# Performance work log

Hardware: AMD Instinct MI355X
Metric: run time of the kernel (lower is better)

Reference implementation:

```python
import jax, jax.numpy as jnp
import numpy as np

N_HEAD = 12


def setup_inputs() -> dict:
    key = jax.random.key(0)
    k1, k2, k3, k4 = jax.random.split(key, 4)
    B, T, C = 2, 2048, 768
    x = jax.random.normal(k1, (B, T, C), jnp.float32)
    eps = 0.1 * jnp.abs(jax.random.normal(k2, (B, T, C), jnp.float32))
    return {
        "x": x,
        "x_lower": x - eps,
        "x_upper": x + eps,
        "W_attn": 0.02 * jax.random.normal(k3, (3 * C, C), jnp.float32),
        "W_proj": 0.02 * jax.random.normal(k4, (C, C), jnp.float32),
    }


def _sdpa(q, k, v):
    # q,k,v: [B,H,T,D]; causal softmax attention
    T = q.shape[-2]
    scale = 1.0 / np.sqrt(q.shape[-1]).astype(np.float32)
    att = jnp.einsum('bhqd,bhkd->bhqk', q, k) * scale
    mask = jnp.tril(jnp.ones((T, T), dtype=bool))
    att = jnp.where(mask, att, -jnp.inf)
    att = jax.nn.softmax(att, axis=-1)
    return jnp.einsum('bhqk,bhkd->bhqd', att, v)


def reference(x, x_lower, x_upper, W_attn, W_proj):
    B, T, C = x.shape
    H = N_HEAD
    D = C // H

    def qkv(inp, W):
        out = inp @ W.T  # [B,T,3C]
        q, k, v = jnp.split(out, 3, axis=-1)
        hd = lambda t: t.reshape(B, T, H, D).transpose(0, 2, 1, 3)
        return hd(q), hd(k), hd(v)

    # nominal path
    q, k, v = qkv(x, W_attn)

    # signed weight split: positive keeps W>=0 entries, negative keeps W<0
    Wp = jnp.maximum(W_attn, 0.0)
    Wn = jnp.minimum(W_attn, 0.0)

    qup, kup, vup = qkv(x_upper, Wp)
    qun, kun, vun = qkv(x_upper, Wn)
    qlp, klp, vlp = qkv(x_lower, Wp)
    qln, kln, vln = qkv(x_lower, Wn)

    q_lo, q_hi = qlp + qun, qup + qln
    k_lo, k_hi = klp + kun, kup + kln
    v_lo, v_hi = vlp + vun, vup + vln

    y = _sdpa(q, k, v)
    # 8 interval-bound SDPA branches (q outer, k mid, v inner: lll..uuu)
    combos = [
        _sdpa(qa, ka, va)
        for qa in (q_lo, q_hi)
        for ka in (k_lo, k_hi)
        for va in (v_lo, v_hi)
    ]
    y_all = jnp.stack(combos, axis=0)  # [8,B,H,T,D]
    y_lo = y_all.min(axis=0)
    y_hi = y_all.max(axis=0)

    merge = lambda t: t.transpose(0, 2, 1, 3).reshape(B, T, C)
    return (merge(y) @ W_proj.T, merge(y_lo) @ W_proj.T, merge(y_hi) @ W_proj.T)
```

## Files before the change

kernel.cpp:

```cpp
#include <hip/hip_runtime.h>
#include <hip/hip_bf16.h>
#include <cstdint>

typedef float f4  __attribute__((ext_vector_type(4)));
typedef short s8v __attribute__((ext_vector_type(8)));
typedef int   i4v __attribute__((ext_vector_type(4)));

#define BHTD 3145728
#define BTC  3145728
#define NT   2048
#define NC   768
#define NWA  1769472
#define NEG  -1e30f
#define QSCALE 0.18033688f

static __device__ __forceinline__ short bfbits(float f) {
    return __builtin_bit_cast(short, __float2bfloat16(f));
}
static __device__ __forceinline__ float bf2f(short s) {
    return __builtin_bit_cast(float, (int)(((unsigned int)(unsigned short)s) << 16));
}
static __device__ __forceinline__ float exp2fast(float x) {
    return __builtin_amdgcn_exp2f(x);
}
static __device__ __forceinline__ int cvtpk_bf16(float lo, float hi) {
    int r;
    asm("v_cvt_pk_bf16_f32 %0, %1, %2" : "=v"(r) : "v"(lo), "v"(hi));
    return r;
}
static __device__ __forceinline__ float rowred_max(float x) {
    x = fmaxf(x, __shfl_xor(x, 16, 64));
    x = fmaxf(x, __shfl_xor(x, 32, 64));
    return x;
}
static __device__ __forceinline__ float rowred_sum(float x) {
    x += __shfl_xor(x, 16, 64);
    x += __shfl_xor(x, 32, 64);
    return x;
}

__global__ __launch_bounds__(256) void prep_cvt(
    const float* __restrict__ x, const float* __restrict__ xl,
    const float* __restrict__ xu, const float* __restrict__ W,
    short* __restrict__ xn, short* __restrict__ xm, short* __restrict__ xr,
    short* __restrict__ wb)
{
    const size_t flat = (size_t)blockIdx.x * 256 + threadIdx.x;
    const size_t i = flat * 8;
    {
        const f4 a0 = *(const f4*)&x[i],  a1 = *(const f4*)&x[i + 4];
        const f4 l0 = *(const f4*)&xl[i], l1 = *(const f4*)&xl[i + 4];
        const f4 u0 = *(const f4*)&xu[i], u1 = *(const f4*)&xu[i + 4];
        s8v vn, vm, vr;
#pragma unroll
        for (int j = 0; j < 4; j++) {
            vn[j]     = bfbits(a0[j]);                   vn[4 + j] = bfbits(a1[j]);
            vm[j]     = bfbits(0.5f * (l0[j] + u0[j]));  vm[4 + j] = bfbits(0.5f * (l1[j] + u1[j]));
            vr[j]     = bfbits(0.5f * (u0[j] - l0[j]));  vr[4 + j] = bfbits(0.5f * (u1[j] - l1[j]));
        }
        *(s8v*)&xn[i] = vn;
        *(s8v*)&xm[i] = vm;
        *(s8v*)&xr[i] = vr;
    }
    if (flat < NWA / 8) {
        const size_t wi = flat * 8;
        const f4 w0 = *(const f4*)&W[wi], w1 = *(const f4*)&W[wi + 4];
        s8v vw;
#pragma unroll
        for (int j = 0; j < 4; j++) { vw[j] = bfbits(w0[j]); vw[4 + j] = bfbits(w1[j]); }
        *(s8v*)&wb[wi] = vw;
    }
}

__global__ __launch_bounds__(256) void qkv_proj_mfma(
    const short* __restrict__ xn, const short* __restrict__ xm,
    const short* __restrict__ xr, const short* __restrict__ wb,
    short* __restrict__ qkvb)
{
    __shared__ short sm[2][4 * 2560];
    short* Eb = &sm[0][0];

    const int b_  = blockIdx.x;
    const int xcd = b_ & 7;
    const int s_  = b_ >> 3;
    const int jx  = s_ % 36;
    const int ny  = xcd + 8 * (s_ / 36);
    const int j0 = jx * 64;
    const int n0 = ny * 64;
    const int t  = threadIdx.x;
    const int wv = t >> 6, lane = t & 63, quad = lane >> 4, l16 = lane & 15;
    const int rw = t >> 2, koff = (t & 3) * 8;

    f4 aN[4], aM[4], aR[4];
#pragma unroll
    for (int i = 0; i < 4; i++) { aN[i] = f4{0,0,0,0}; aM[i] = f4{0,0,0,0}; aR[i] = f4{0,0,0,0}; }

    const size_t abase = (size_t)(n0 + rw) * NC + koff;
    const size_t bbase = (size_t)(j0 + rw) * NC + koff;

    s8v rn, rm, rr, rb;
    rn = *(const s8v*)&xn[abase];
    rm = *(const s8v*)&xm[abase];
    rr = *(const s8v*)&xr[abase];
    rb = *(const s8v*)&wb[bbase];
    *(s8v*)&sm[0][rw * 40 + koff]        = rn;
    *(s8v*)&sm[0][2560 + rw * 40 + koff] = rm;
    *(s8v*)&sm[0][5120 + rw * 40 + koff] = rr;
    *(s8v*)&sm[0][7680 + rw * 40 + koff] = rb;

    for (int it = 0; it < NC / 32; ++it) {
        const int cb = it & 1, nb = cb ^ 1;
        __syncthreads();
        const bool pf = (it + 1 < NC / 32);
        if (pf) {
            const size_t k1 = (size_t)(it + 1) * 32;
            rn = *(const s8v*)&xn[abase + k1];
            rm = *(const s8v*)&xm[abase + k1];
            rr = *(const s8v*)&xr[abase + k1];
            rb = *(const s8v*)&wb[bbase + k1];
        }
        const s8v fx = *(const s8v*)&sm[cb][(wv * 16 + l16) * 40 + quad * 8];
        const s8v fm = *(const s8v*)&sm[cb][2560 + (wv * 16 + l16) * 40 + quad * 8];
        const s8v fr = *(const s8v*)&sm[cb][5120 + (wv * 16 + l16) * 40 + quad * 8];
#pragma unroll
        for (int nt = 0; nt < 4; ++nt) {
            const s8v fb = *(const s8v*)&sm[cb][7680 + (nt * 16 + l16) * 40 + quad * 8];
            i4v bi = __builtin_bit_cast(i4v, fb);
#pragma unroll
            for (int i = 0; i < 4; i++) bi[i] &= 0x7fff7fff;
            const s8v fa = __builtin_bit_cast(s8v, bi);
            aN[nt] = __builtin_amdgcn_mfma_f32_16x16x32_bf16(fx, fb, aN[nt], 0, 0, 0);
            aM[nt] = __builtin_amdgcn_mfma_f32_16x16x32_bf16(fm, fb, aM[nt], 0, 0, 0);
            aR[nt] = __builtin_amdgcn_mfma_f32_16x16x32_bf16(fr, fa, aR[nt], 0, 0, 0);
        }
        if (pf) {
            *(s8v*)&sm[nb][rw * 40 + koff]        = rn;
            *(s8v*)&sm[nb][2560 + rw * 40 + koff] = rm;
            *(s8v*)&sm[nb][5120 + rw * 40 + koff] = rr;
            *(s8v*)&sm[nb][7680 + rw * 40 + koff] = rb;
        }
    }

    const int p = j0 / NC, hh = (j0 % NC) >> 6;
    const float osc = (p == 0) ? QSCALE : 1.0f;
    const int cc16 = (t & 3) * 16;
    for (int var = 0; var < 3; ++var) {
        __syncthreads();
#pragma unroll
        for (int nt = 0; nt < 4; ++nt)
#pragma unroll
            for (int r = 0; r < 4; ++r) {
                const float v = (var == 0) ? aN[nt][r]
                              : (var == 1) ? aM[nt][r] - aR[nt][r]
                                           : aM[nt][r] + aR[nt][r];
                Eb[(wv * 16 + quad * 4 + r) * 72 + nt * 16 + l16] = bfbits(v * osc);
            }
        __syncthreads();
        short* dst = qkvb + (size_t)(var * 3 + p) * BHTD;
        if (p < 2) {
            const int token = n0 + rw, b = token >> 11, tt = token & 2047;
            const size_t o = ((size_t)(b * 12 + hh) * NT + tt) * 64 + cc16;
            *(s8v*)&dst[o]     = *(const s8v*)&Eb[rw * 72 + cc16];
            *(s8v*)&dst[o + 8] = *(const s8v*)&Eb[rw * 72 + cc16 + 8];
        } else {
            const int d = rw;
            s8v e0, e1;
#pragma unroll
            for (int i = 0; i < 8; i++) e0[i] = Eb[(cc16 + i) * 72 + d];
#pragma unroll
            for (int i = 0; i < 8; i++) e1[i] = Eb[(cc16 + 8 + i) * 72 + d];
            const int token0 = n0 + cc16, b = token0 >> 11, tt = token0 & 2047;
            const size_t o = ((size_t)(b * 12 + hh) * 64 + d) * NT + tt;
            *(s8v*)&dst[o]     = e0;
            *(s8v*)&dst[o + 8] = e1;
        }
    }
}

__global__ __launch_bounds__(256) void flash_mfma(
    const short* __restrict__ qkvb, float* __restrict__ ybuf,
    short* __restrict__ cand)
{
    const int b_  = blockIdx.x;
    const int xcd = b_ & 7;
    const int r_  = b_ >> 3;
    const int pr  = r_ & 7;
    const int r2  = r_ >> 3;
    const int z   = r2 % 5;
    const int bh  = xcd + 8 * (r2 / 5);
    const int t   = threadIdx.x;
    const int wv = t >> 6, lane = t & 63, quad = lane >> 4, l16 = lane & 15;
    const bool TWO = (z != 0);

    __shared__ short Ks[2][32 * 70];
    __shared__ short Vs[2][2][64 * 40];

    int sv, qvi, kvi, v0i, v1i;
    if (TWO) { sv = z; qvi = (sv + 1) >> 1; kvi = 2 - (sv & 1); v0i = 1; v1i = 2; }
    else     { sv = 0; qvi = 0; kvi = 0; v0i = 0; v1i = 0; }

    const size_t hb = (size_t)bh * (NT * 64);
    const short* Qp  = qkvb + (size_t)(qvi * 3 + 0) * BHTD + hb;
    const short* Kp  = qkvb + (size_t)(kvi * 3 + 1) * BHTD + hb;
    const short* V0p = qkvb + (size_t)(v0i * 3 + 2) * BHTD + hb;
    const short* V1p = qkvb + (size_t)(v1i * 3 + 2) * BHTD + hb;

    const int skr = t >> 3, skc = (t & 7) * 8;
    const int svd = t >> 2, svc = (t & 3) * 8;
    const int sig = (l16 >> 2) * 8 + (l16 & 3);

    for (int half = 0; half < 2; ++half) {
        const int qt = half ? (15 - pr) : pr;
        const int q0 = qt * 128;

        s8v qf[2][2];
#pragma unroll
        for (int mt = 0; mt < 2; ++mt)
#pragma unroll
            for (int ch = 0; ch < 2; ++ch)
                qf[mt][ch] = *(const s8v*)&Qp[(size_t)(q0 + 32 * wv + 16 * mt + l16) * 64 + ch * 32 + quad * 8];

        float mi[2], li[2];
        mi[0] = mi[1] = NEG; li[0] = li[1] = 0.f;
        f4 acc0[2][4], acc1[2][4];
#pragma unroll
        for (int mt = 0; mt < 2; ++mt)
#pragma unroll
            for (int i = 0; i < 4; ++i) { acc0[mt][i] = f4{0,0,0,0}; acc1[mt][i] = f4{0,0,0,0}; }

        const int ktn  = 4 * qt + 4;
        const int mykt = 4 * qt + wv + 1;

        __syncthreads();
        s8v rK, rV0, rV1;
        rK  = *(const s8v*)&Kp[(size_t)skr * 64 + skc];
        rV0 = *(const s8v*)&V0p[(size_t)svd * NT + svc];
        if (TWO) rV1 = *(const s8v*)&V1p[(size_t)svd * NT + svc];
        *(s8v*)&Ks[0][skr * 70 + skc]    = rK;
        *(s8v*)&Vs[0][0][svd * 40 + svc] = rV0;
        if (TWO) *(s8v*)&Vs[0][1][svd * 40 + svc] = rV1;

        for (int kt = 0; kt < ktn; ++kt) {
            const int k0 = kt * 32;
            const int cb = kt & 1, nb = cb ^ 1;
            __syncthreads();
            const bool pf = (kt + 1 < ktn);
            if (pf) {
                const int k1 = k0 + 32;
                rK  = *(const s8v*)&Kp[(size_t)(k1 + skr) * 64 + skc];
                rV0 = *(const s8v*)&V0p[(size_t)svd * NT + k1 + svc];
                if (TWO) rV1 = *(const s8v*)&V1p[(size_t)svd * NT + k1 + svc];
            }
            if (kt < mykt) {
                f4 s[2][2];
#pragma unroll
                for (int mt = 0; mt < 2; ++mt) { s[mt][0] = f4{0,0,0,0}; s[mt][1] = f4{0,0,0,0}; }
                __builtin_amdgcn_s_setprio(1);
#pragma unroll
                for (int nt = 0; nt < 2; ++nt)
#pragma unroll
                    for (int ch = 0; ch < 2; ++ch) {
                        const s8v kf = *(const s8v*)&Ks[cb][(sig + nt * 4) * 70 + ch * 32 + quad * 8];
                        s[0][nt] = __builtin_amdgcn_mfma_f32_16x16x32_bf16(kf, qf[0][ch], s[0][nt], 0, 0, 0);
                        s[1][nt] = __builtin_amdgcn_mfma_f32_16x16x32_bf16(kf, qf[1][ch], s[1][nt], 0, 0, 0);
                    }
                __builtin_amdgcn_s_setprio(0);

                s8v pa[2];
#pragma unroll
                for (int mt = 0; mt < 2; ++mt) {
                    const int rowb = q0 + 32 * wv + 16 * mt;
                    const int qrow = rowb + l16;
                    float a[8];
#pragma unroll
                    for (int nt = 0; nt < 2; ++nt)
#pragma unroll
                        for (int r = 0; r < 4; ++r) a[nt * 4 + r] = s[mt][nt][r];
                    if (k0 + 31 > rowb) {
#pragma unroll
                        for (int nt = 0; nt < 2; ++nt)
#pragma unroll
                            for (int r = 0; r < 4; ++r)
                                if (k0 + quad * 8 + nt * 4 + r > qrow) a[nt * 4 + r] = NEG;
                    }
                    const float c = fmaxf(fmaxf(fmaxf(a[0], a[1]), fmaxf(a[2], a[3])),
                                          fmaxf(fmaxf(a[4], a[5]), fmaxf(a[6], a[7])));
                    if (__any(c - mi[mt] > 8.0f)) {
                        const float mx = rowred_max(c);
                        const float nm = fmaxf(mi[mt], mx);
                        const float al = exp2fast(mi[mt] - nm);
                        mi[mt] = nm;
                        li[mt] *= al;
#pragma unroll
                        for (int r = 0; r < 4; ++r) {
                            const float alr = __shfl(al, (lane & 48) | (quad * 4 + r), 64);
#pragma unroll
                            for (int dt = 0; dt < 4; ++dt) acc0[mt][dt][r] *= alr;
                            if (TWO) {
#pragma unroll
                                for (int dt = 0; dt < 4; ++dt) acc1[mt][dt][r] *= alr;
                            }
                        }
                    }
                    float p[8];
#pragma unroll
                    for (int j = 0; j < 8; ++j) p[j] = exp2fast(a[j] - mi[mt]);
                    li[mt] += ((p[0] + p[1]) + (p[2] + p[3])) + ((p[4] + p[5]) + (p[6] + p[7]));
                    i4v pi;
#pragma unroll
                    for (int jj = 0; jj < 4; ++jj)
                        pi[jj] = cvtpk_bf16(p[2 * jj], p[2 * jj + 1]);
                    pa[mt] = __builtin_bit_cast(s8v, pi);
                }
                __builtin_amdgcn_s_setprio(1);
#pragma unroll
                for (int dt = 0; dt < 4; ++dt) {
                    const s8v vf0 = *(const s8v*)&Vs[cb][0][(dt * 16 + l16) * 40 + quad * 8];
                    acc0[0][dt] = __builtin_amdgcn_mfma_f32_16x16x32_bf16(pa[0], vf0, acc0[0][dt], 0, 0, 0);
                    acc0[1][dt] = __builtin_amdgcn_mfma_f32_16x16x32_bf16(pa[1], vf0, acc0[1][dt], 0, 0, 0);
                    if (TWO) {
                        const s8v vf1 = *(const s8v*)&Vs[cb][1][(dt * 16 + l16) * 40 + quad * 8];
                        acc1[0][dt] = __builtin_amdgcn_mfma_f32_16x16x32_bf16(pa[0], vf1, acc1[0][dt], 0, 0, 0);
                        acc1[1][dt] = __builtin_amdgcn_mfma_f32_16x16x32_bf16(pa[1], vf1, acc1[1][dt], 0, 0, 0);
                    }
                }
                __builtin_amdgcn_s_setprio(0);
            }
            if (pf) {
                *(s8v*)&Ks[nb][skr * 70 + skc]    = rK;
                *(s8v*)&Vs[nb][0][svd * 40 + svc] = rV0;
                if (TWO) *(s8v*)&Vs[nb][1][svd * 40 + svc] = rV1;
            }
        }

#pragma unroll
        for (int mt = 0; mt < 2; ++mt) {
            const float invq = 1.f / rowred_sum(li[mt]);
            float inv[4];
#pragma unroll
            for (int r = 0; r < 4; ++r)
                inv[r] = __shfl(invq, (lane & 48) | (quad * 4 + r), 64);
#pragma unroll
            for (int dt = 0; dt < 4; ++dt)
#pragma unroll
                for (int r = 0; r < 4; ++r) {
                    const size_t o = hb + (size_t)(q0 + 32 * wv + 16 * mt + quad * 4 + r) * 64 + dt * 16 + l16;
                    if (!TWO) {
                        ybuf[o] = acc0[mt][dt][r] * inv[r];
                    } else {
                        const float xa = acc0[mt][dt][r] * inv[r];
                        const float xb = acc1[mt][dt][r] * inv[r];
                        cand[(size_t)(sv - 1) * BHTD + o] = bfbits(fminf(xa, xb));
                        cand[(size_t)(3 + sv) * BHTD + o] = bfbits(fmaxf(xa, xb));
                    }
                }
        }
    }
}

__global__ __launch_bounds__(256) void out_proj_mfma(
    const float* __restrict__ ybuf, const short* __restrict__ cand,
    const float* __restrict__ Wp, float* __restrict__ out)
{
    __shared__ short sm3[2][2 * 2560];
    float* Eb = (float*)sm3;

    const int b_  = blockIdx.x;
    const int xcd = b_ & 7;
    const int s_  = b_ >> 3;
    const int o   = s_ % 3;
    const int jx  = (s_ / 3) % 12;
    const int ny  = xcd + 8 * (s_ / 36);
    const int j0 = jx * 64, n0 = ny * 64;
    const int t  = threadIdx.x;
    const int wv = t >> 6, lane = t & 63, quad = lane >> 4, l16 = lane & 15;
    const int rw = t >> 2, koff = (t & 3) * 8;

    f4 acc[4];
#pragma unroll
    for (int i = 0; i < 4; i++) acc[i] = f4{0,0,0,0};

    const int token = n0 + rw, b = token >> 11, tt = token & 2047;
    const size_t wbase = (size_t)(j0 + rw) * NC + koff;
    const short* cb = cand + (size_t)(o == 1 ? 0 : 4) * BHTD;

    f4 ry0, ry1, rw0, rw1;
    s8v rc0, rc1, rc2, rc3;

    auto convert = [&](s8v& av, s8v& bv) {
        if (o == 0) {
#pragma unroll
            for (int i = 0; i < 4; i++) { av[i] = bfbits(ry0[i]); av[4 + i] = bfbits(ry1[i]); }
        } else {
            float v[8];
#pragma unroll
            for (int i = 0; i < 8; i++) v[i] = bf2f(rc0[i]);
            if (o == 1) {
#pragma unroll
                for (int i = 0; i < 8; i++) v[i] = fminf(v[i], bf2f(rc1[i]));
#pragma unroll
                for (int i = 0; i < 8; i++) v[i] = fminf(v[i], bf2f(rc2[i]));
#pragma unroll
                for (int i = 0; i < 8; i++) v[i] = fminf(v[i], bf2f(rc3[i]));
            } else {
#pragma unroll
                for (int i = 0; i < 8; i++) v[i] = fmaxf(v[i], bf2f(rc1[i]));
#pragma unroll
                for (int i = 0; i < 8; i++) v[i] = fmaxf(v[i], bf2f(rc2[i]));
#pragma unroll
                for (int i = 0; i < 8; i++) v[i] = fmaxf(v[i], bf2f(rc3[i]));
            }
#pragma unroll
            for (int i = 0; i < 8; i++) av[i] = bfbits(v[i]);
        }
#pragma unroll
        for (int i = 0; i < 4; i++) { bv[i] = bfbits(rw0[i]); bv[4 + i] = bfbits(rw1[i]); }
    };
    auto loadTile = [&](int k1) {
        const int hh = k1 >> 6, d0 = (k1 & 63) + koff;
        const size_t aoff = ((size_t)(b * 12 + hh) * NT + tt) * 64 + d0;
        if (o == 0) {
            ry0 = *(const f4*)&ybuf[aoff];
            ry1 = *(const f4*)&ybuf[aoff + 4];
        } else {
            rc0 = *(const s8v*)&cb[aoff];
            rc1 = *(const s8v*)&cb[(size_t)1 * BHTD + aoff];
            rc2 = *(const s8v*)&cb[(size_t)2 * BHTD + aoff];
            rc3 = *(const s8v*)&cb[(size_t)3 * BHTD + aoff];
        }
        rw0 = *(const f4*)&Wp[wbase + k1];
        rw1 = *(const f4*)&Wp[wbase + k1 + 4];
    };

    loadTile(0);
    {
        s8v av, bv;
        convert(av, bv);
        *(s8v*)&sm3[0][rw * 40 + koff]        = av;
        *(s8v*)&sm3[0][2560 + rw * 40 + koff] = bv;
    }

    for (int it = 0; it < NC / 32; ++it) {
        const int cbuf = it & 1, nbuf = cbuf ^ 1;
        __syncthreads();
        const bool pf = (it + 1 < NC / 32);
        if (pf) loadTile((it + 1) * 32);
        const s8v af = *(const s8v*)&sm3[cbuf][(wv * 16 + l16) * 40 + quad * 8];
#pragma unroll
        for (int nt = 0; nt < 4; ++nt) {
            const s8v bf = *(const s8v*)&sm3[cbuf][2560 + (nt * 16 + l16) * 40 + quad * 8];
            acc[nt] = __builtin_amdgcn_mfma_f32_16x16x32_bf16(af, bf, acc[nt], 0, 0, 0);
        }
        if (pf) {
            s8v av, bv;
            convert(av, bv);
            *(s8v*)&sm3[nbuf][rw * 40 + koff]        = av;
            *(s8v*)&sm3[nbuf][2560 + rw * 40 + koff] = bv;
        }
    }
    __syncthreads();
#pragma unroll
    for (int nt = 0; nt < 4; ++nt)
#pragma unroll
        for (int r = 0; r < 4; ++r)
            Eb[(wv * 16 + quad * 4 + r) * 68 + nt * 16 + l16] = acc[nt][r];
    __syncthreads();
    const int cc = (t & 3) * 16;
#pragma unroll
    for (int i = 0; i < 4; ++i) {
        const f4 vo = *(const f4*)&Eb[rw * 68 + cc + 4 * i];
        *(f4*)&out[(size_t)o * BTC + (size_t)(n0 + rw) * NC + j0 + cc + 4 * i] = vo;
    }
}

extern "C" void kernel_launch(void* const* d_in, const int* in_sizes, int n_in,
                              void* d_out, int out_size, void* d_ws, size_t ws_size,
                              hipStream_t stream)
{
    const float* x  = (const float*)d_in[0];
    const float* xl = (const float*)d_in[1];
    const float* xu = (const float*)d_in[2];
    const float* Wa = (const float*)d_in[3];
    const float* Wp = (const float*)d_in[4];
    float* out = (float*)d_out;

    short* qkvb = (short*)d_ws;
    float* ybuf = (float*)(qkvb + (size_t)9 * BHTD);
    short* cand = (short*)(ybuf + (size_t)BHTD);

    short* xn = cand;
    short* xm = cand + (size_t)1 * BHTD;
    short* xr = cand + (size_t)2 * BHTD;
    short* wb = cand + (size_t)3 * BHTD;

    prep_cvt     <<<dim3(1536), 256, 0, stream>>>(x, xl, xu, Wa, xn, xm, xr, wb);
    qkv_proj_mfma<<<dim3(2304), 256, 0, stream>>>(xn, xm, xr, wb, qkvb);
    flash_mfma   <<<dim3(960),  256, 0, stream>>>(qkvb, ybuf, cand);
    out_proj_mfma<<<dim3(2304), 256, 0, stream>>>(ybuf, cand, Wp, out);
}
```

Baseline: 417.8 us.

## Pre-reduce interval candidates and pre-convert out-proj operands to bf16

Adds a prep_out kernel that reduces the four min and four max candidate buffers into single bf16 lo/hi buffers in place. The nominal attention output is stored as bf16, and W_proj is converted to bf16 in the prep kernel. The output projection then loads one bf16 A tile and a bf16 B tile with no per-tile conversion. This removes redundant 4-way candidate reads repeated across column blocks, at the cost of an extra kernel launch and pass.

```diff
diff --git a/kernel.cpp b/kernel.cpp
--- a/kernel.cpp
+++ b/kernel.cpp
@@ -11,6 +11,7 @@
 #define NT   2048
 #define NC   768
 #define NWA  1769472
+#define NWP  589824
 #define NEG  -1e30f
 #define QSCALE 0.18033688f
 
@@ -42,8 +43,9 @@
 __global__ __launch_bounds__(256) void prep_cvt(
     const float* __restrict__ x, const float* __restrict__ xl,
     const float* __restrict__ xu, const float* __restrict__ W,
+    const float* __restrict__ Wp,
     short* __restrict__ xn, short* __restrict__ xm, short* __restrict__ xr,
-    short* __restrict__ wb)
+    short* __restrict__ wb, short* __restrict__ wpb)
 {
     const size_t flat = (size_t)blockIdx.x * 256 + threadIdx.x;
     const size_t i = flat * 8;
@@ -69,6 +71,14 @@
 #pragma unroll
         for (int j = 0; j < 4; j++) { vw[j] = bfbits(w0[j]); vw[4 + j] = bfbits(w1[j]); }
         *(s8v*)&wb[wi] = vw;
+    }
+    if (flat < NWP / 8) {
+        const size_t wi = flat * 8;
+        const f4 w0 = *(const f4*)&Wp[wi], w1 = *(const f4*)&Wp[wi + 4];
+        s8v vw;
+#pragma unroll
+        for (int j = 0; j < 4; j++) { vw[j] = bfbits(w0[j]); vw[4 + j] = bfbits(w1[j]); }
+        *(s8v*)&wpb[wi] = vw;
     }
 }
 
@@ -178,7 +188,7 @@
 }
 
 __global__ __launch_bounds__(256) void flash_mfma(
-    const short* __restrict__ qkvb, float* __restrict__ ybuf,
+    const short* __restrict__ qkvb, short* __restrict__ ybf,
     short* __restrict__ cand)
 {
     const int b_  = blockIdx.x;
@@ -346,7 +356,7 @@
                 for (int r = 0; r < 4; ++r) {
                     const size_t o = hb + (size_t)(q0 + 32 * wv + 16 * mt + quad * 4 + r) * 64 + dt * 16 + l16;
                     if (!TWO) {
-                        ybuf[o] = acc0[mt][dt][r] * inv[r];
+                        ybf[o] = bfbits(acc0[mt][dt][r] * inv[r]);
                     } else {
                         const float xa = acc0[mt][dt][r] * inv[r];
                         const float xb = acc1[mt][dt][r] * inv[r];
@@ -358,9 +368,42 @@
     }
 }
 
+__global__ __launch_bounds__(256) void prep_out(short* __restrict__ cand)
+{
+    const size_t i = ((size_t)blockIdx.x * 256 + threadIdx.x) * 8;
+    {
+        const s8v c0 = *(const s8v*)&cand[i];
+        const s8v c1 = *(const s8v*)&cand[(size_t)1 * BHTD + i];
+        const s8v c2 = *(const s8v*)&cand[(size_t)2 * BHTD + i];
+        const s8v c3 = *(const s8v*)&cand[(size_t)3 * BHTD + i];
+        s8v lo;
+#pragma unroll
+        for (int j = 0; j < 8; j++) {
+            const float v = fminf(fminf(bf2f(c0[j]), bf2f(c1[j])),
+                                  fminf(bf2f(c2[j]), bf2f(c3[j])));
+            lo[j] = (short)(__builtin_bit_cast(unsigned int, v) >> 16);
+        }
+        *(s8v*)&cand[i] = lo;
+    }
+    {
+        const s8v c0 = *(const s8v*)&cand[(size_t)4 * BHTD + i];
+        const s8v c1 = *(const s8v*)&cand[(size_t)5 * BHTD + i];
+        const s8v c2 = *(const s8v*)&cand[(size_t)6 * BHTD + i];
+        const s8v c3 = *(const s8v*)&cand[(size_t)7 * BHTD + i];
+        s8v hi;
+#pragma unroll
+        for (int j = 0; j < 8; j++) {
+            const float v = fmaxf(fmaxf(bf2f(c0[j]), bf2f(c1[j])),
+                                  fmaxf(bf2f(c2[j]), bf2f(c3[j])));
+            hi[j] = (short)(__builtin_bit_cast(unsigned int, v) >> 16);
+        }
+        *(s8v*)&cand[(size_t)4 * BHTD + i] = hi;
+    }
+}
+
 __global__ __launch_bounds__(256) void out_proj_mfma(
-    const float* __restrict__ ybuf, const short* __restrict__ cand,
-    const float* __restrict__ Wp, float* __restrict__ out)
+    const short* __restrict__ ybf, const short* __restrict__ cand,
+    const short* __restrict__ wpb, float* __restrict__ out)
 {
     __shared__ short sm3[2][2 * 2560];
     float* Eb = (float*)sm3;
@@ -382,63 +425,19 @@
 
     const int token = n0 + rw, b = token >> 11, tt = token & 2047;
     const size_t wbase = (size_t)(j0 + rw) * NC + koff;
-    const short* cb = cand + (size_t)(o == 1 ? 0 : 4) * BHTD;
-
-    f4 ry0, ry1, rw0, rw1;
-    s8v rc0, rc1, rc2, rc3;
-
-    auto convert = [&](s8v& av, s8v& bv) {
-        if (o == 0) {
-#pragma unroll
-            for (int i = 0; i < 4; i++) { av[i] = bfbits(ry0[i]); av[4 + i] = bfbits(ry1[i]); }
-        } else {
-            float v[8];
-#pragma unroll
-            for (int i = 0; i < 8; i++) v[i] = bf2f(rc0[i]);
-            if (o == 1) {
-#pragma unroll
-                for (int i = 0; i < 8; i++) v[i] = fminf(v[i], bf2f(rc1[i]));
-#pragma unroll
-                for (int i = 0; i < 8; i++) v[i] = fminf(v[i], bf2f(rc2[i]));
-#pragma unroll
-                for (int i = 0; i < 8; i++) v[i] = fminf(v[i], bf2f(rc3[i]));
-            } else {
-#pragma unroll
-                for (int i = 0; i < 8; i++) v[i] = fmaxf(v[i], bf2f(rc1[i]));
-#pragma unroll
-                for (int i = 0; i < 8; i++) v[i] = fmaxf(v[i], bf2f(rc2[i]));
-#pragma unroll
-                for (int i = 0; i < 8; i++) v[i] = fmaxf(v[i], bf2f(rc3[i]));
-            }
-#pragma unroll
-            for (int i = 0; i < 8; i++) av[i] = bfbits(v[i]);
-        }
-#pragma unroll
-        for (int i = 0; i < 4; i++) { bv[i] = bfbits(rw0[i]); bv[4 + i] = bfbits(rw1[i]); }
-    };
+    const short* Ap = (o == 0) ? ybf : (o == 1) ? cand : cand + (size_t)4 * BHTD;
+
+    s8v ra, rb;
     auto loadTile = [&](int k1) {
         const int hh = k1 >> 6, d0 = (k1 & 63) + koff;
         const size_t aoff = ((size_t)(b * 12 + hh) * NT + tt) * 64 + d0;
-        if (o == 0) {
-            ry0 = *(const f4*)&ybuf[aoff];
-            ry1 = *(const f4*)&ybuf[aoff + 4];
-        } else {
-            rc0 = *(const s8v*)&cb[aoff];
-            rc1 = *(const s8v*)&cb[(size_t)1 * BHTD + aoff];
-            rc2 = *(const s8v*)&cb[(size_t)2 * BHTD + aoff];
-            rc3 = *(const s8v*)&cb[(size_t)3 * BHTD + aoff];
-        }
-        rw0 = *(const f4*)&Wp[wbase + k1];
-        rw1 = *(const f4*)&Wp[wbase + k1 + 4];
+        ra = *(const s8v*)&Ap[aoff];
+        rb = *(const s8v*)&wpb[wbase + k1];
     };
 
     loadTile(0);
-    {
-        s8v av, bv;
-        convert(av, bv);
-        *(s8v*)&sm3[0][rw * 40 + koff]        = av;
-        *(s8v*)&sm3[0][2560 + rw * 40 + koff] = bv;
-    }
+    *(s8v*)&sm3[0][rw * 40 + koff]        = ra;
+    *(s8v*)&sm3[0][2560 + rw * 40 + koff] = rb;
 
     for (int it = 0; it < NC / 32; ++it) {
         const int cbuf = it & 1, nbuf = cbuf ^ 1;
@@ -452,10 +451,8 @@
             acc[nt] = __builtin_amdgcn_mfma_f32_16x16x32_bf16(af, bf, acc[nt], 0, 0, 0);
         }
         if (pf) {
-            s8v av, bv;
-            convert(av, bv);
-            *(s8v*)&sm3[nbuf][rw * 40 + koff]        = av;
-            *(s8v*)&sm3[nbuf][2560 + rw * 40 + koff] = bv;
+            *(s8v*)&sm3[nbuf][rw * 40 + koff]        = ra;
+            *(s8v*)&sm3[nbuf][2560 + rw * 40 + koff] = rb;
         }
     }
     __syncthreads();
@@ -485,16 +482,18 @@
     float* out = (float*)d_out;
 
     short* qkvb = (short*)d_ws;
-    float* ybuf = (float*)(qkvb + (size_t)9 * BHTD);
-    short* cand = (short*)(ybuf + (size_t)BHTD);
+    short* ybf  = qkvb + (size_t)9 * BHTD;
+    short* cand = ybf + (size_t)BHTD;
+    short* wpb  = cand + (size_t)8 * BHTD;
 
     short* xn = cand;
     short* xm = cand + (size_t)1 * BHTD;
     short* xr = cand + (size_t)2 * BHTD;
     short* wb = cand + (size_t)3 * BHTD;
 
-    prep_cvt     <<<dim3(1536), 256, 0, stream>>>(x, xl, xu, Wa, xn, xm, xr, wb);
+    prep_cvt     <<<dim3(1536), 256, 0, stream>>>(x, xl, xu, Wa, Wp, xn, xm, xr, wb, wpb);
     qkv_proj_mfma<<<dim3(2304), 256, 0, stream>>>(xn, xm, xr, wb, qkvb);
-    flash_mfma   <<<dim3(960),  256, 0, stream>>>(qkvb, ybuf, cand);
-    out_proj_mfma<<<dim3(2304), 256, 0, stream>>>(ybuf, cand, Wp, out);
-}
+    flash_mfma   <<<dim3(960),  256, 0, stream>>>(qkvb, ybf, cand);
+    prep_out     <<<dim3(1536), 256, 0, stream>>>(cand);
+    out_proj_mfma<<<dim3(2304), 256, 0, stream>>>(ybf, cand, wpb, out);
+}
```

After: 396.6 us. -5.1%, faster.
